# Optimization experiments

Measured on AMD Instinct MI355X. Metric: run time of the kernel, lower is better.

## Reference

```python
import jax, jax.numpy as jnp
import numpy as np

B, S, D, H = 2, 2048, 2048, 16
HD = D // H          # 128
HALF = HD // 2       # 64
EPS = 1e-6


def setup_inputs() -> dict:
    key = jax.random.key(0)
    ks = jax.random.split(key, 10)
    x = jax.random.normal(ks[0], (B, S, D), jnp.float32)
    # RoPE frequencies: standard theta=10000, per (position, half head dim)
    inv_freq = 1.0 / (10000.0 ** (np.arange(HALF, dtype=np.float64) / HALF))
    ang = np.outer(np.arange(S, dtype=np.float64), inv_freq)  # (S, HALF)
    freqs_cos = jnp.asarray(np.cos(ang), jnp.float32)[:, None, :]  # (S,1,HALF)
    freqs_sin = jnp.asarray(np.sin(ang), jnp.float32)[:, None, :]
    sc = 0.02
    qw = jax.random.normal(ks[1], (D, D), jnp.float32) * sc
    kw = jax.random.normal(ks[2], (D, D), jnp.float32) * sc
    vw = jax.random.normal(ks[3], (D, D), jnp.float32) * sc
    ow = jax.random.normal(ks[4], (D, D), jnp.float32) * sc
    qb = jax.random.normal(ks[5], (D,), jnp.float32) * sc
    kb = jax.random.normal(ks[6], (D,), jnp.float32) * sc
    vb = jax.random.normal(ks[7], (D,), jnp.float32) * sc
    ob = jax.random.normal(ks[8], (D,), jnp.float32) * sc
    qnorm_w = jnp.ones((D,), jnp.float32)
    knorm_w = jnp.ones((D,), jnp.float32)
    return {"x": x, "freqs_cos": freqs_cos, "freqs_sin": freqs_sin,
            "qw": qw, "qb": qb, "kw": kw, "kb": kb, "vw": vw, "vb": vb,
            "ow": ow, "ob": ob, "qnorm_w": qnorm_w, "knorm_w": knorm_w}


def _rmsnorm(h, w):
    # norm in fp32 over full last dim (dim, not per-head), as in the source
    hf = h.astype(jnp.float32)
    inv = jax.lax.rsqrt(jnp.mean(hf * hf, axis=-1, keepdims=True) + EPS)
    return (hf * inv).astype(h.dtype) * w


def _rope(h, cos, sin):
    # h: (B,S,D) -> complex rotation on interleaved pairs per head
    b, s, _ = h.shape
    hp = h.reshape(b, s, H, HALF, 2)
    x1, x2 = hp[..., 0], hp[..., 1]
    c = cos[None]   # (1,S,1,HALF) broadcasts over batch & heads
    sn = sin[None]
    o1 = x1 * c - x2 * sn
    o2 = x1 * sn + x2 * c
    return jnp.stack([o1, o2], axis=-1).reshape(b, s, H * HD)


def reference(x, freqs_cos, freqs_sin, qw, qb, kw, kb, vw, vb, ow, ob, qnorm_w, knorm_w):
    q = _rope(_rmsnorm(x @ qw.T + qb, qnorm_w), freqs_cos, freqs_sin)
    k = _rope(_rmsnorm(x @ kw.T + kb, knorm_w), freqs_cos, freqs_sin)
    v = x @ vw.T + vb
    b, s, _ = x.shape
    qh = q.reshape(b, s, H, HD)
    kh = k.reshape(b, s, H, HD)
    vh = v.reshape(b, s, H, HD)
    scale = 1.0 / jnp.sqrt(jnp.float32(HD))
    att = jnp.einsum('bqhd,bkhd->bhqk', qh, kh) * scale
    p = jax.nn.softmax(att, axis=-1)
    o = jnp.einsum('bhqk,bkhd->bqhd', p, vh).reshape(b, s, D)
    return o @ ow.T + ob
```

## Files before the change

kernel.cpp:

```cpp
#include <hip/hip_runtime.h>
#include <stdint.h>

#define B_SZ 2
#define S_LEN 2048
#define D_DIM 2048
#define NHEAD 16
#define HD 128
#define HALF 64
#define MROWS (B_SZ * S_LEN)

typedef __attribute__((ext_vector_type(8))) __bf16 bf16x8;
typedef __attribute__((ext_vector_type(8))) unsigned short u16x8;
typedef __attribute__((ext_vector_type(4))) float f32x4;
typedef __attribute__((ext_vector_type(16))) float f32x16;
typedef __attribute__((ext_vector_type(4))) unsigned int u32x4;

__device__ inline unsigned short f2bf(float x) {
  union { float f; uint32_t u; } c; c.f = x;
  uint32_t r = (c.u + 0x7fffu + ((c.u >> 16) & 1u)) >> 16;
  return (unsigned short)r;
}

__device__ inline float bf2f(unsigned short b) {
  union { uint32_t u; float f; } c; c.u = (uint32_t)b << 16;
  return c.f;
}

__device__ inline void gll16(const void* g, void* l) {
  __builtin_amdgcn_global_load_lds(
      (const __attribute__((address_space(1))) void*)g,
      (__attribute__((address_space(3))) void*)l,
      16, 0, 0);
}

__global__ void cast_all(const float* __restrict__ x,
                         const float* __restrict__ qw, const float* __restrict__ kw,
                         const float* __restrict__ vw, const float* __restrict__ ow,
                         unsigned short* __restrict__ xb,
                         unsigned short* __restrict__ qwb, unsigned short* __restrict__ kwb,
                         unsigned short* __restrict__ vwb, unsigned short* __restrict__ owb) {
  const int n_x = (MROWS * D_DIM) / 4;
  const int n_w = (D_DIM * D_DIM) / 4;
  const int total = n_x + 4 * n_w;
  int i = blockIdx.x * blockDim.x + threadIdx.x;
  int stride = gridDim.x * blockDim.x;
  for (; i < total; i += stride) {
    const float* src; unsigned short* dst; int off;
    if (i < n_x) { src = x; dst = xb; off = i; }
    else {
      int j = i - n_x;
      int seg = j >> 20;
      off = j & (n_w - 1);
      src = seg == 0 ? qw : seg == 1 ? kw : seg == 2 ? vw : ow;
      dst = seg == 0 ? qwb : seg == 1 ? kwb : seg == 2 ? vwb : owb;
    }
    float4 v = reinterpret_cast<const float4*>(src)[off];
    ushort4 o;
    o.x = f2bf(v.x); o.y = f2bf(v.y); o.z = f2bf(v.z); o.w = f2bf(v.w);
    reinterpret_cast<ushort4*>(dst)[off] = o;
  }
}

template <int MODE>
__global__ __launch_bounds__(256) void gemm_bt(
    const unsigned short* __restrict__ A, const unsigned short* __restrict__ Bt,
    const float* __restrict__ bias, void* __restrict__ C0,
    unsigned short* __restrict__ C1, unsigned short* __restrict__ C2,
    int M, int N, int K) {
  __shared__ __align__(16) unsigned short As[128 * 64];
  __shared__ __align__(16) unsigned short Bs[128 * 64];
  const int tid = threadIdx.x;
  const int lane = tid & 63;
  const int wave = tid >> 6;
  const int nbn = N >> 7;
  const int xcd = blockIdx.x & 7;
  const int w = blockIdx.x >> 3;
  const int bm = w & 31;
  const int bn = xcd * (nbn >> 3) + (w >> 5);
  const int wr = wave >> 1, wc = wave & 1;
  const int lm = lane & 15, lg = lane >> 4;

  f32x4 acc[4][4] = {};

  for (int k0 = 0; k0 < K; k0 += 64) {
    __syncthreads();
#pragma unroll
    for (int r = 0; r < 4; ++r) {
      int p = r * 4096 + tid * 16;
      int row = p >> 7;
      int ch = (p >> 4) & 7;
      int sc = (ch ^ (row & 7)) << 3;
      gll16(A + (size_t)(bm * 128 + row) * K + k0 + sc, (char*)As + p);
      gll16(Bt + (size_t)(bn * 128 + row) * K + k0 + sc, (char*)Bs + p);
    }
    __syncthreads();

#pragma unroll
    for (int kk = 0; kk < 2; ++kk) {
      bf16x8 af[4], bfr[4];
#pragma unroll
      for (int mi = 0; mi < 4; ++mi) {
        int row = wr * 64 + mi * 16 + lm;
        af[mi] = *reinterpret_cast<const bf16x8*>(
            (const char*)As + row * 128 + ((((kk << 2) + lg) ^ (row & 7)) << 4));
      }
#pragma unroll
      for (int ni = 0; ni < 4; ++ni) {
        int row = wc * 64 + ni * 16 + lm;
        bfr[ni] = *reinterpret_cast<const bf16x8*>(
            (const char*)Bs + row * 128 + ((((kk << 2) + lg) ^ (row & 7)) << 4));
      }
#pragma unroll
      for (int mi = 0; mi < 4; ++mi)
#pragma unroll
        for (int ni = 0; ni < 4; ++ni)
          acc[mi][ni] = __builtin_amdgcn_mfma_f32_16x16x32_bf16(
              af[mi], bfr[ni], acc[mi][ni], 0, 0, 0);
    }
  }

#pragma unroll
  for (int ni = 0; ni < 4; ++ni) {
    int col = bn * 128 + wc * 64 + ni * 16 + lm;
    float bv = bias[col];
    if constexpr (MODE == 3) {
      int seg = col >> 11;
      int c2 = col & (D_DIM - 1);
#pragma unroll
      for (int mi = 0; mi < 4; ++mi) {
        int row0 = bm * 128 + wr * 64 + mi * 16 + lg * 4;
        if (seg == 2) {
          int b = row0 >> 11, s0 = row0 & (S_LEN - 1);
          int h = c2 >> 7, d = c2 & (HD - 1);
          ushort4 o;
          o.x = f2bf(acc[mi][ni][0] + bv);
          o.y = f2bf(acc[mi][ni][1] + bv);
          o.z = f2bf(acc[mi][ni][2] + bv);
          o.w = f2bf(acc[mi][ni][3] + bv);
          size_t oi = ((((size_t)(b * NHEAD + h) * (S_LEN / 64) + (s0 >> 6)) * HD + d) << 6)
                      + (s0 & 63);
          *reinterpret_cast<ushort4*>(C2 + oi) = o;
        } else {
          unsigned short* dst = (seg == 0) ? (unsigned short*)C0 : C1;
#pragma unroll
          for (int r = 0; r < 4; ++r)
            dst[(size_t)(row0 + r) * D_DIM + c2] = f2bf(acc[mi][ni][r] + bv);
        }
      }
    } else {
      float* out = (float*)C0;
#pragma unroll
      for (int mi = 0; mi < 4; ++mi) {
        int row0 = bm * 128 + wr * 64 + mi * 16 + lg * 4;
#pragma unroll
        for (int r = 0; r < 4; ++r)
          out[(size_t)(row0 + r) * N + col] = acc[mi][ni][r] + bv;
      }
    }
  }
}

__global__ __launch_bounds__(256) void norm_rope2(
    const unsigned short* __restrict__ qin, const unsigned short* __restrict__ kin,
    const float* __restrict__ qnw, const float* __restrict__ knw,
    const float* __restrict__ cosb, const float* __restrict__ sinb,
    unsigned short* __restrict__ qout, unsigned short* __restrict__ kout,
    float qscale) {
  const int isK = blockIdx.x >> 12;
  const int row = blockIdx.x & (MROWS - 1);
  const int pos = row & (S_LEN - 1);
  const unsigned short* hr = (isK ? kin : qin) + (size_t)row * D_DIM;
  const float* w = isK ? knw : qnw;
  const float outscale = isK ? 1.0f : qscale;
  const int t = threadIdx.x;
  const int d = t * 8;

  u16x8 hv = *reinterpret_cast<const u16x8*>(hr + d);
  float a[8];
#pragma unroll
  for (int i = 0; i < 8; ++i) a[i] = bf2f(hv[i]);
  float ss = 0.f;
#pragma unroll
  for (int i = 0; i < 8; ++i) ss += a[i] * a[i];
#pragma unroll
  for (int off = 32; off > 0; off >>= 1) ss += __shfl_down(ss, off);
  __shared__ float red[4];
  if ((t & 63) == 0) red[t >> 6] = ss;
  __syncthreads();
  float tot = red[0] + red[1] + red[2] + red[3];
  float inv = rsqrtf(tot * (1.0f / D_DIM) + 1e-6f) * outscale;

  const int p = (d & (HD - 1)) >> 1;
  const float* cp = cosb + pos * HALF + p;
  const float* sp = sinb + pos * HALF + p;
  const float* wp = w + d;

  float c0 = cp[0], c1 = cp[1], c2 = cp[2], c3 = cp[3];
  float s0 = sp[0], s1 = sp[1], s2 = sp[2], s3 = sp[3];
#pragma unroll
  for (int i = 0; i < 8; ++i) a[i] = a[i] * inv * wp[i];
  u16x8 o;
  o[0] = f2bf(a[0] * c0 - a[1] * s0);
  o[1] = f2bf(a[0] * s0 + a[1] * c0);
  o[2] = f2bf(a[2] * c1 - a[3] * s1);
  o[3] = f2bf(a[2] * s1 + a[3] * c1);
  o[4] = f2bf(a[4] * c2 - a[5] * s2);
  o[5] = f2bf(a[4] * s2 + a[5] * c2);
  o[6] = f2bf(a[6] * c3 - a[7] * s3);
  o[7] = f2bf(a[6] * s3 + a[7] * c3);
  if (isK) {
    int hh = t >> 4;
    int dd = d & (HD - 1);
    size_t oi = (((size_t)((row >> 11) * NHEAD + hh) * S_LEN) + pos) * HD + dd;
    *reinterpret_cast<u16x8*>(kout + oi) = o;
  } else {
    *reinterpret_cast<u16x8*>(qout + (size_t)row * D_DIM + d) = o;
  }
}

__global__ __launch_bounds__(512) void attn_kernel(
    const unsigned short* __restrict__ Q, const unsigned short* __restrict__ Kh,
    const unsigned short* __restrict__ Vt, unsigned short* __restrict__ O) {
  const int idx = blockIdx.x;
  const int swz = (idx & 7) * 32 + (idx >> 3);
  const int qb = swz & 7;
  const int h = (swz >> 3) & 15;
  const int b = swz >> 7;

  const int tid = threadIdx.x;
  const int lane = tid & 63;
  const int wave = tid >> 6;
  const int l31 = lane & 31;
  const int hh = lane >> 5;

  const size_t qbase = (size_t)b * S_LEN * D_DIM + (size_t)h * HD;
  const size_t hbase = (size_t)(b * NHEAD + h) * S_LEN * HD;
  const int q0w = qb * 256 + wave * 32;

  __shared__ __align__(16) unsigned short Ks[2 * 128 * 128];
  __shared__ __align__(16) unsigned short Vs[2 * 128 * 64];

  bf16x8 qf[8];
#pragma unroll
  for (int ds_ = 0; ds_ < 8; ++ds_)
    qf[ds_] = *reinterpret_cast<const bf16x8*>(
        Q + qbase + (size_t)(q0w + l31) * D_DIM + ds_ * 16 + hh * 8);

  f32x16 oacc[4] = {};
  float mrow = -1e30f, lrow = 0.f;

  const int pbase = wave * 1024 + (lane << 4);

  auto stageK = [&](int buf, int tix) {
    const unsigned short* ksrc = Kh + hbase + (size_t)tix * (128 * HD);
#pragma unroll
    for (int j = 0; j < 4; ++j) {
      int p = pbase + j * 8192;
      int kr = p >> 8;
      int kc = ((p >> 4) & 15) ^ ((kr & 7) ^ ((kr >> 3) & 7));
      gll16(ksrc + kr * 128 + kc * 8, (char*)Ks + buf * 32768 + p);
    }
  };
  auto stageV = [&](int tix) {
    const unsigned short* vsrc = Vt + hbase + (size_t)tix * (128 * HD);
#pragma unroll
    for (int j = 0; j < 4; ++j) {
      int p = pbase + j * 8192;
      int vr = (p & 16383) >> 7;
      int vc = ((p >> 4) & 7) ^ (((vr & 7) ^ ((vr >> 3) & 7)) & 7);
      gll16(vsrc + (p >> 14) * (64 * HD) + vr * 64 + vc * 8, (char*)Vs + p);
    }
  };

  stageK(0, 0);

  const int NT = S_LEN / 128;
  for (int t = 0; t < NT; ++t) {
    const int cur = t & 1;
    stageV(t);
    stageK(cur ^ 1, (t + 1 < NT) ? t + 1 : t);
    asm volatile("s_waitcnt vmcnt(8)" ::: "memory");
    __builtin_amdgcn_sched_barrier(0);
    __builtin_amdgcn_s_barrier();
    __builtin_amdgcn_sched_barrier(0);

    const char* kbp = (const char*)Ks + cur * 32768;
    f32x16 sc[4] = {};
    __builtin_amdgcn_s_setprio(1);
#pragma unroll
    for (int ds_ = 0; ds_ < 8; ++ds_) {
#pragma unroll
      for (int j = 0; j < 4; ++j) {
        int r = j * 32 + l31;
        bf16x8 kf = *reinterpret_cast<const bf16x8*>(
            kbp + r * 256 + (((ds_ * 2 + hh) ^ ((r & 7) ^ ((r >> 3) & 7))) << 4));
        sc[j] = __builtin_amdgcn_mfma_f32_32x32x16_bf16(kf, qf[ds_], sc[j], 0, 0, 0);
      }
    }
    __builtin_amdgcn_s_setprio(0);

    float m0[16];
#pragma unroll
    for (int r = 0; r < 16; ++r)
      m0[r] = fmaxf(fmaxf(sc[0][r], sc[1][r]), fmaxf(sc[2][r], sc[3][r]));
#pragma unroll
    for (int r = 0; r < 8; ++r) m0[r] = fmaxf(m0[r], m0[r + 8]);
#pragma unroll
    for (int r = 0; r < 4; ++r) m0[r] = fmaxf(m0[r], m0[r + 4]);
    float mx = fmaxf(fmaxf(m0[0], m0[1]), fmaxf(m0[2], m0[3]));
    mx = fmaxf(mx, __shfl_xor(mx, 32));
    if (__any(mx > mrow + 8.0f)) {
      float nm = fmaxf(mrow, mx);
      float alpha = exp2f(mrow - nm);
      mrow = nm;
      lrow *= alpha;
#pragma unroll
      for (int r = 0; r < 16; ++r) {
        int qr = (r & 3) + 8 * (r >> 2) + 4 * hh;
        float av = __shfl(alpha, qr);
        oacc[0][r] *= av; oacc[1][r] *= av; oacc[2][r] *= av; oacc[3][r] *= av;
      }
    }
#pragma unroll
    for (int j = 0; j < 4; ++j)
#pragma unroll
      for (int r = 0; r < 16; ++r) sc[j][r] = exp2f(sc[j][r] - mrow);
    float s0[16];
#pragma unroll
    for (int r = 0; r < 16; ++r)
      s0[r] = (sc[0][r] + sc[1][r]) + (sc[2][r] + sc[3][r]);
#pragma unroll
    for (int r = 0; r < 8; ++r) s0[r] += s0[r + 8];
#pragma unroll
    for (int r = 0; r < 4; ++r) s0[r] += s0[r + 4];
    lrow += (s0[0] + s0[1]) + (s0[2] + s0[3]);

    uint32_t w[32];
#pragma unroll
    for (int X = 0; X < 4; ++X) {
#pragma unroll
      for (int g = 0; g < 4; ++g) {
        uint32_t lo, hi;
        float a0 = sc[X][4 * g], a1 = sc[X][4 * g + 1];
        float a2 = sc[X][4 * g + 2], a3 = sc[X][4 * g + 3];
        asm("v_cvt_pk_bf16_f32 %0, %1, %2" : "=v"(lo) : "v"(a0), "v"(a1));
        asm("v_cvt_pk_bf16_f32 %0, %1, %2" : "=v"(hi) : "v"(a2), "v"(a3));
        w[X * 8 + g * 2] = lo; w[X * 8 + g * 2 + 1] = hi;
      }
    }
    bf16x8 pa[8];
#pragma unroll
    for (int s = 0; s < 8; ++s) {
      int wb = (s >> 1) * 8 + (s & 1) * 4;
      uint32_t le = w[wb], he = w[wb + 1], lo_ = w[wb + 2], ho = w[wb + 3];
      asm("v_permlane32_swap_b32 %0, %1" : "+v"(le), "+v"(lo_));
      asm("v_permlane32_swap_b32 %0, %1" : "+v"(he), "+v"(ho));
      u32x4 fr = {le, he, lo_, ho};
      pa[s] = __builtin_bit_cast(bf16x8, fr);
    }

    asm volatile("s_waitcnt vmcnt(4)" ::: "memory");
    __builtin_amdgcn_sched_barrier(0);
    __builtin_amdgcn_s_barrier();
    __builtin_amdgcn_sched_barrier(0);

    const char* vbp = (const char*)Vs;
    __builtin_amdgcn_s_setprio(1);
#pragma unroll
    for (int db = 0; db < 4; ++db) {
      int d = db * 32 + l31;
      int fv = ((d & 7) ^ ((d >> 3) & 7)) & 7;
#pragma unroll
      for (int ks = 0; ks < 8; ++ks) {
        bf16x8 vv = *reinterpret_cast<const bf16x8*>(
            vbp + (ks >> 2) * 16384 + d * 128 + ((((ks & 3) * 2 + hh) ^ fv) << 4));
        oacc[db] = __builtin_amdgcn_mfma_f32_32x32x16_bf16(pa[ks], vv, oacc[db], 0, 0, 0);
      }
    }
    __builtin_amdgcn_s_setprio(0);

    __builtin_amdgcn_sched_barrier(0);
    __builtin_amdgcn_s_barrier();
    __builtin_amdgcn_sched_barrier(0);
  }

  lrow += __shfl_xor(lrow, 32);
  float inv_[16];
#pragma unroll
  for (int r = 0; r < 16; ++r) {
    int qr = (r & 3) + 8 * (r >> 2) + 4 * hh;
    inv_[r] = 1.0f / __shfl(lrow, qr);
  }
#pragma unroll
  for (int db = 0; db < 4; ++db) {
#pragma unroll
    for (int r = 0; r < 16; ++r) {
      int qr = (r & 3) + 8 * (r >> 2) + 4 * hh;
      O[qbase + (size_t)(q0w + qr) * D_DIM + db * 32 + l31] =
          f2bf(oacc[db][r] * inv_[r]);
    }
  }
}

extern "C" void kernel_launch(void* const* d_in, const int* in_sizes, int n_in,
                              void* d_out, int out_size, void* d_ws, size_t ws_size,
                              hipStream_t stream) {
  const float* x   = (const float*)d_in[0];
  const float* fc  = (const float*)d_in[1];
  const float* fs  = (const float*)d_in[2];
  const float* qw  = (const float*)d_in[3];
  const float* qb  = (const float*)d_in[4];
  const float* kw  = (const float*)d_in[5];
  const float* kb  = (const float*)d_in[6];
  const float* vw  = (const float*)d_in[7];
  const float* vb  = (const float*)d_in[8];
  const float* ow  = (const float*)d_in[9];
  const float* ob  = (const float*)d_in[10];
  const float* qnw = (const float*)d_in[11];
  const float* knw = (const float*)d_in[12];
  float* out = (float*)d_out;

  const size_t MSD = (size_t)MROWS * D_DIM;
  const size_t WSZ = (size_t)D_DIM * D_DIM;
  char* ws = (char*)d_ws;
  unsigned short* xb   = (unsigned short*)ws; ws += MSD * 2;
  unsigned short* qwb  = (unsigned short*)ws; ws += WSZ * 2;
  unsigned short* kwb  = (unsigned short*)ws; ws += WSZ * 2;
  unsigned short* vwb  = (unsigned short*)ws; ws += WSZ * 2;
  unsigned short* owb  = (unsigned short*)ws; ws += WSZ * 2;
  float*          cbias = (float*)ws;         ws += 3 * D_DIM * 4;
  unsigned short* qpre = (unsigned short*)ws; ws += MSD * 2;
  unsigned short* kpre = (unsigned short*)ws; ws += MSD * 2;
  unsigned short* qb16 = (unsigned short*)ws; ws += MSD * 2;
  unsigned short* kb16 = (unsigned short*)ws; ws += MSD * 2;
  unsigned short* vt16 = (unsigned short*)ws; ws += MSD * 2;
  unsigned short* ob16 = (unsigned short*)ws; ws += MSD * 2;

  cast_all<<<2048, 256, 0, stream>>>(x, qw, kw, vw, ow, xb, qwb, kwb, vwb, owb);
  hipMemcpyAsync(cbias,              qb, D_DIM * sizeof(float), hipMemcpyDeviceToDevice, stream);
  hipMemcpyAsync(cbias + D_DIM,      kb, D_DIM * sizeof(float), hipMemcpyDeviceToDevice, stream);
  hipMemcpyAsync(cbias + 2 * D_DIM,  vb, D_DIM * sizeof(float), hipMemcpyDeviceToDevice, stream);

  gemm_bt<3><<<dim3((MROWS / 128) * (3 * D_DIM / 128)), 256, 0, stream>>>(
      xb, qwb, cbias, qpre, kpre, vt16, MROWS, 3 * D_DIM, D_DIM);

  const float qscale = 0.08838834764831845f * 1.4426950408889634f;
  norm_rope2<<<2 * MROWS, 256, 0, stream>>>(qpre, kpre, qnw, knw, fc, fs,
                                            qb16, kb16, qscale);

  attn_kernel<<<dim3(S_LEN / 256 * NHEAD * B_SZ), 512, 0, stream>>>(qb16, kb16, vt16, ob16);

  gemm_bt<0><<<dim3((MROWS / 128) * (D_DIM / 128)), 256, 0, stream>>>(
      ob16, owb, ob, out, nullptr, nullptr, MROWS, D_DIM, D_DIM);
}
```

Baseline: 291.9 us.

## Use 256x256 double-buffered 8-wave GEMM for fused QKV projection

Replaces the 128x128 single-buffered QKV GEMM with a new 512-thread kernel that computes 256x256 output tiles. It double-buffers LDS and interleaves the async global-to-LDS loads for the next K step with four quadrant MFMA phases separated by barriers. The larger tile halves global traffic per FLOP and overlaps loads with compute. In exchange it uses more LDS (128KB) and more accumulator registers, which lowers occupancy. The output-projection GEMM keeps the old kernel, stripped of its template mode.

```diff
diff --git a/kernel.cpp b/kernel.cpp
--- a/kernel.cpp
+++ b/kernel.cpp
@@ -32,6 +32,8 @@
       (__attribute__((address_space(3))) void*)l,
       16, 0, 0);
 }
+
+#define SB __builtin_amdgcn_sched_barrier(0)
 
 __global__ void cast_all(const float* __restrict__ x,
                          const float* __restrict__ qw, const float* __restrict__ kw,
@@ -61,11 +63,146 @@
   }
 }
 
-template <int MODE>
+__global__ __launch_bounds__(512) void gemm256q(
+    const unsigned short* __restrict__ A, const unsigned short* __restrict__ Bt,
+    const float* __restrict__ bias, unsigned short* __restrict__ C0,
+    unsigned short* __restrict__ C1, unsigned short* __restrict__ C2,
+    int M, int N, int K) {
+  __shared__ __align__(16) unsigned short Asq[2 * 2 * 128 * 64];
+  __shared__ __align__(16) unsigned short Bsq[2 * 2 * 128 * 64];
+  const int tid = threadIdx.x;
+  const int lane = tid & 63;
+  const int wave = tid >> 6;
+  const int wr = wave >> 2;
+  const int wc = wave & 3;
+  const int lm = lane & 15, lg = lane >> 4;
+  const int xcd = blockIdx.x & 7;
+  const int w = blockIdx.x >> 3;
+  const int bm = w & 15;
+  const int bn = xcd * ((N >> 8) >> 3) + (w >> 4);
+
+  const int pb0 = tid * 16, pb1 = tid * 16 + 8192;
+  const int r0 = pb0 >> 7, s0_ = (((pb0 >> 4) & 7) ^ (r0 & 7)) << 3;
+  const int r1 = pb1 >> 7, s1_ = (((pb1 >> 4) & 7) ^ (r1 & 7)) << 3;
+  const unsigned short* A00 = A + (size_t)(bm * 256 + r0) * K + s0_;
+  const unsigned short* A01 = A + (size_t)(bm * 256 + r1) * K + s1_;
+  const unsigned short* A10 = A + (size_t)(bm * 256 + 128 + r0) * K + s0_;
+  const unsigned short* A11 = A + (size_t)(bm * 256 + 128 + r1) * K + s1_;
+  const unsigned short* B00 = Bt + (size_t)(bn * 256 + r0) * K + s0_;
+  const unsigned short* B01 = Bt + (size_t)(bn * 256 + r1) * K + s1_;
+  const unsigned short* B10 = Bt + (size_t)(bn * 256 + 128 + r0) * K + s0_;
+  const unsigned short* B11 = Bt + (size_t)(bn * 256 + 128 + r1) * K + s1_;
+
+  f32x4 acc[8][4] = {};
+
+#define LOADQ(KK, MQ, AF, BF)                                                  \
+  _Pragma("unroll") for (int i = 0; i < 4; ++i) {                              \
+    int rra = (MQ)*64 + i * 16 + lm;                                           \
+    AF[i] = *reinterpret_cast<const bf16x8*>((const char*)Asq + cur * 32768 +  \
+        wr * 16384 + rra * 128 + ((((KK)*4 + lg) ^ (rra & 7)) << 4));          \
+  }                                                                            \
+  _Pragma("unroll") for (int j = 0; j < 4; ++j) {                              \
+    int rrb = (wc & 1) * 64 + j * 16 + lm;                                     \
+    BF[j] = *reinterpret_cast<const bf16x8*>((const char*)Bsq + cur * 32768 +  \
+        (wc >> 1) * 16384 + rrb * 128 + ((((KK)*4 + lg) ^ (rrb & 7)) << 4));   \
+  }
+
+#define MFMA16(MQ, AF, BF)                                                     \
+  __builtin_amdgcn_s_setprio(1);                                               \
+  _Pragma("unroll") for (int i = 0; i < 4; ++i)                                \
+    _Pragma("unroll") for (int j = 0; j < 4; ++j)                              \
+      acc[(MQ)*4 + i][j] = __builtin_amdgcn_mfma_f32_16x16x32_bf16(            \
+          AF[i], BF[j], acc[(MQ)*4 + i][j], 0, 0, 0);                          \
+  __builtin_amdgcn_s_setprio(0)
+
+#define BARRIER  SB; __builtin_amdgcn_s_barrier(); SB
+
+  const int NT = K >> 6;
+  gll16(A00, (char*)Asq + pb0);          gll16(A01, (char*)Asq + pb1);
+  gll16(A10, (char*)Asq + 16384 + pb0);  gll16(A11, (char*)Asq + 16384 + pb1);
+  gll16(B00, (char*)Bsq + pb0);          gll16(B01, (char*)Bsq + pb1);
+  gll16(B10, (char*)Bsq + 16384 + pb0);  gll16(B11, (char*)Bsq + 16384 + pb1);
+
+  for (int t = 0; t < NT; ++t) {
+    const int cur = t & 1;
+    const int sb = (cur ^ 1) * 32768;
+    const int koff = ((t + 1 < NT) ? t + 1 : t) << 6;
+
+    gll16(A00 + koff, (char*)Asq + sb + pb0);
+    gll16(A01 + koff, (char*)Asq + sb + pb1);
+    asm volatile("s_waitcnt vmcnt(2)" ::: "memory");
+    BARRIER;
+    {
+      bf16x8 af[4], bf[4];
+      LOADQ(0, 0, af, bf);
+      MFMA16(0, af, bf);
+    }
+    BARRIER;
+    {
+      bf16x8 af[4], bf[4];
+      LOADQ(0, 1, af, bf);
+      gll16(A10 + koff, (char*)Asq + sb + 16384 + pb0);
+      gll16(A11 + koff, (char*)Asq + sb + 16384 + pb1);
+      BARRIER;
+      MFMA16(1, af, bf);
+    }
+    BARRIER;
+    {
+      bf16x8 af[4], bf[4];
+      LOADQ(1, 0, af, bf);
+      gll16(B00 + koff, (char*)Bsq + sb + pb0);
+      gll16(B01 + koff, (char*)Bsq + sb + pb1);
+      BARRIER;
+      MFMA16(0, af, bf);
+    }
+    BARRIER;
+    {
+      bf16x8 af[4], bf[4];
+      LOADQ(1, 1, af, bf);
+      gll16(B10 + koff, (char*)Bsq + sb + 16384 + pb0);
+      gll16(B11 + koff, (char*)Bsq + sb + 16384 + pb1);
+      BARRIER;
+      MFMA16(1, af, bf);
+    }
+    BARRIER;
+  }
+#undef LOADQ
+#undef MFMA16
+#undef BARRIER
+
+#pragma unroll
+  for (int nf = 0; nf < 4; ++nf) {
+    int col = bn * 256 + wc * 64 + nf * 16 + lm;
+    float bv = bias[col];
+    int seg = col >> 11;
+    int c2 = col & (D_DIM - 1);
+#pragma unroll
+    for (int mf = 0; mf < 8; ++mf) {
+      int row0 = bm * 256 + wr * 128 + mf * 16 + lg * 4;
+      if (seg == 2) {
+        int b = row0 >> 11, sp = row0 & (S_LEN - 1);
+        int h = c2 >> 7, d = c2 & (HD - 1);
+        ushort4 o;
+        o.x = f2bf(acc[mf][nf][0] + bv);
+        o.y = f2bf(acc[mf][nf][1] + bv);
+        o.z = f2bf(acc[mf][nf][2] + bv);
+        o.w = f2bf(acc[mf][nf][3] + bv);
+        size_t oi = ((((size_t)(b * NHEAD + h) * (S_LEN / 64) + (sp >> 6)) * HD + d) << 6)
+                    + (sp & 63);
+        *reinterpret_cast<ushort4*>(C2 + oi) = o;
+      } else {
+        unsigned short* dst = (seg == 0) ? C0 : C1;
+#pragma unroll
+        for (int r = 0; r < 4; ++r)
+          dst[(size_t)(row0 + r) * D_DIM + c2] = f2bf(acc[mf][nf][r] + bv);
+      }
+    }
+  }
+}
+
 __global__ __launch_bounds__(256) void gemm_bt(
     const unsigned short* __restrict__ A, const unsigned short* __restrict__ Bt,
-    const float* __restrict__ bias, void* __restrict__ C0,
-    unsigned short* __restrict__ C1, unsigned short* __restrict__ C2,
+    const float* __restrict__ bias, float* __restrict__ C0,
     int M, int N, int K) {
   __shared__ __align__(16) unsigned short As[128 * 64];
   __shared__ __align__(16) unsigned short Bs[128 * 64];
@@ -123,39 +260,12 @@
   for (int ni = 0; ni < 4; ++ni) {
     int col = bn * 128 + wc * 64 + ni * 16 + lm;
     float bv = bias[col];
-    if constexpr (MODE == 3) {
-      int seg = col >> 11;
-      int c2 = col & (D_DIM - 1);
-#pragma unroll
-      for (int mi = 0; mi < 4; ++mi) {
-        int row0 = bm * 128 + wr * 64 + mi * 16 + lg * 4;
-        if (seg == 2) {
-          int b = row0 >> 11, s0 = row0 & (S_LEN - 1);
-          int h = c2 >> 7, d = c2 & (HD - 1);
-          ushort4 o;
-          o.x = f2bf(acc[mi][ni][0] + bv);
-          o.y = f2bf(acc[mi][ni][1] + bv);
-          o.z = f2bf(acc[mi][ni][2] + bv);
-          o.w = f2bf(acc[mi][ni][3] + bv);
-          size_t oi = ((((size_t)(b * NHEAD + h) * (S_LEN / 64) + (s0 >> 6)) * HD + d) << 6)
-                      + (s0 & 63);
-          *reinterpret_cast<ushort4*>(C2 + oi) = o;
-        } else {
-          unsigned short* dst = (seg == 0) ? (unsigned short*)C0 : C1;
-#pragma unroll
-          for (int r = 0; r < 4; ++r)
-            dst[(size_t)(row0 + r) * D_DIM + c2] = f2bf(acc[mi][ni][r] + bv);
-        }
-      }
-    } else {
-      float* out = (float*)C0;
-#pragma unroll
-      for (int mi = 0; mi < 4; ++mi) {
-        int row0 = bm * 128 + wr * 64 + mi * 16 + lg * 4;
-#pragma unroll
-        for (int r = 0; r < 4; ++r)
-          out[(size_t)(row0 + r) * N + col] = acc[mi][ni][r] + bv;
-      }
+#pragma unroll
+    for (int mi = 0; mi < 4; ++mi) {
+      int row0 = bm * 128 + wr * 64 + mi * 16 + lg * 4;
+#pragma unroll
+      for (int r = 0; r < 4; ++r)
+        C0[(size_t)(row0 + r) * N + col] = acc[mi][ni][r] + bv;
     }
   }
 }
@@ -280,9 +390,9 @@
     stageV(t);
     stageK(cur ^ 1, (t + 1 < NT) ? t + 1 : t);
     asm volatile("s_waitcnt vmcnt(8)" ::: "memory");
-    __builtin_amdgcn_sched_barrier(0);
+    SB;
     __builtin_amdgcn_s_barrier();
-    __builtin_amdgcn_sched_barrier(0);
+    SB;
 
     const char* kbp = (const char*)Ks + cur * 32768;
     f32x16 sc[4] = {};
@@ -360,9 +470,9 @@
     }
 
     asm volatile("s_waitcnt vmcnt(4)" ::: "memory");
-    __builtin_amdgcn_sched_barrier(0);
+    SB;
     __builtin_amdgcn_s_barrier();
-    __builtin_amdgcn_sched_barrier(0);
+    SB;
 
     const char* vbp = (const char*)Vs;
     __builtin_amdgcn_s_setprio(1);
@@ -379,9 +489,9 @@
     }
     __builtin_amdgcn_s_setprio(0);
 
-    __builtin_amdgcn_sched_barrier(0);
+    SB;
     __builtin_amdgcn_s_barrier();
-    __builtin_amdgcn_sched_barrier(0);
+    SB;
   }
 
   lrow += __shfl_xor(lrow, 32);
@@ -441,7 +551,7 @@
   hipMemcpyAsync(cbias + D_DIM,      kb, D_DIM * sizeof(float), hipMemcpyDeviceToDevice, stream);
   hipMemcpyAsync(cbias + 2 * D_DIM,  vb, D_DIM * sizeof(float), hipMemcpyDeviceToDevice, stream);
 
-  gemm_bt<3><<<dim3((MROWS / 128) * (3 * D_DIM / 128)), 256, 0, stream>>>(
+  gemm256q<<<dim3((MROWS / 256) * (3 * D_DIM / 256)), 512, 0, stream>>>(
       xb, qwb, cbias, qpre, kpre, vt16, MROWS, 3 * D_DIM, D_DIM);
 
   const float qscale = 0.08838834764831845f * 1.4426950408889634f;
@@ -450,6 +560,6 @@
 
   attn_kernel<<<dim3(S_LEN / 256 * NHEAD * B_SZ), 512, 0, stream>>>(qb16, kb16, vt16, ob16);
 
-  gemm_bt<0><<<dim3((MROWS / 128) * (D_DIM / 128)), 256, 0, stream>>>(
-      ob16, owb, ob, out, nullptr, nullptr, MROWS, D_DIM, D_DIM);
-}
+  gemm_bt<<<dim3((MROWS / 128) * (D_DIM / 128)), 256, 0, stream>>>(
+      ob16, owb, ob, out, MROWS, D_DIM, D_DIM);
+}
```

Result: slower. 310.7 us (+6.4%).
